# Kernel optimization log

Hardware: AMD Instinct MI355X
Metric: run time of the kernel (lower is better)

## Reference

```python
import jax, jax.numpy as jnp
import numpy as np

B, S, QW, HID, HEADS = 1, 4096, 512, 512, 8
D = HID // HEADS  # size_per_head = 64
SCALE = 1.0 / np.sqrt(float(D))


def setup_inputs() -> dict:
    key = jax.random.key(0)
    k1, k2, k3, k4, k5 = jax.random.split(key, 5)
    return {
        "tensor_q": jax.random.normal(k1, (B, S, QW), dtype=jnp.float32),
        "tensor_k": jax.random.normal(k2, (B, S, QW), dtype=jnp.float32),
        "tensor_v": jax.random.normal(k3, (B, S, QW), dtype=jnp.float32),
        # in_proj_layer: [3*hidden, q_width] (torch uses rand uniform init; randn fine for reference)
        "in_proj": jax.random.normal(k4, (3 * HID, QW), dtype=jnp.float32) * 0.02,
        # out_proj: nn.Linear(hidden, out, bias=False) weight shape [out, hidden]
        "w_out": jax.random.normal(k5, (HID, HID), dtype=jnp.float32) * 0.02,
    }


def reference(tensor_q, tensor_k, tensor_v, in_proj, w_out):
    b, s, _ = tensor_q.shape
    wq, wk, wv = in_proj[:HID], in_proj[HID:2 * HID], in_proj[2 * HID:]
    # mm(W, x_2d^T)^T  ==  x_2d @ W^T ; reshape to [b, s, heads, d]
    q = (tensor_q.reshape(-1, QW) @ wq.T).reshape(b, s, HEADS, D)
    k = (tensor_k.reshape(-1, QW) @ wk.T).reshape(b, s, HEADS, D)
    v = (tensor_v.reshape(-1, QW) @ wv.T).reshape(b, s, HEADS, D)
    # scores: [b, h, s_q, s_k], explicitly materialized as in the source
    scores = jnp.einsum('bqhd,bkhd->bhqk', q, k) * SCALE
    probs = jax.nn.softmax(scores, axis=-1)
    ctx = jnp.einsum('bhqk,bkhd->bqhd', probs, v).reshape(b * s, HID)
    out = ctx @ w_out.T
    return out.reshape(b, s, HID)
```

## Files before the change

kernel.cpp:

```cpp
#include <hip/hip_runtime.h>
#include <hip/hip_bf16.h>

#define S_LEN 4096
#define QW_K  512
#define HID_N 512
#define HEADS 8
#define DH    64
#define QSCALE (0.125f * 1.4426950408889634f)

typedef _Float16 f16;
typedef _Float16 half8  __attribute__((ext_vector_type(8)));
typedef _Float16 half4v __attribute__((ext_vector_type(4)));
typedef float    float4v __attribute__((ext_vector_type(4)));
typedef float    f32x16 __attribute__((ext_vector_type(16)));
typedef unsigned int uint;
typedef unsigned int uint4v __attribute__((ext_vector_type(4)));

__device__ inline uint pkh(float a, float b) {
    return __builtin_bit_cast(uint, __builtin_amdgcn_cvt_pkrtz(a, b));
}
__device__ inline void plswap(uint& a, uint& b) {
    asm volatile("v_permlane32_swap_b32 %0, %1" : "+v"(a), "+v"(b));
}
__device__ inline float hexp2(float x) {
    float r;
    asm("v_exp_f32 %0, %1" : "=v"(r) : "v"(x));
    return r;
}
__device__ __forceinline__ int swz(int s) {
    return (s & 56) | ((s ^ (s >> 3)) & 7);
}


__global__ __launch_bounds__(256) void proj_kernel(
    const float* __restrict__ xq, const float* __restrict__ xk,
    const float* __restrict__ xv, const float* __restrict__ in_proj,
    f16* __restrict__ qws, f16* __restrict__ kws, f16* __restrict__ vtws)
{
    __shared__ f16 As[128][40];
    __shared__ f16 Ws[128][40];

    const int tid  = threadIdx.x;
    const int lane = tid & 63;
    const int w    = tid >> 6;
    const int wm   = w >> 1, wn = w & 1;
    const int l15  = lane & 15, g = lane >> 4;
    const int m0   = blockIdx.x * 128;
    const int n0   = blockIdx.y * 128;
    const int matid = n0 >> 9;
    const float* A = (matid == 0) ? xq : (matid == 1) ? xk : xv;

    float4v acc[4][4];
    for (int i = 0; i < 4; i++)
        for (int j = 0; j < 4; j++)
            for (int r = 0; r < 4; r++) acc[i][j][r] = 0.0f;

    const int srow = tid >> 3;
    const int scol = (tid & 7) * 4;

    for (int k0 = 0; k0 < QW_K; k0 += 32) {
        __syncthreads();
        #pragma unroll
        for (int p = 0; p < 4; p++) {
            int r = p * 32 + srow;
            float4v av = *(const float4v*)(A + (size_t)(m0 + r) * QW_K + k0 + scol);
            float4v wv = *(const float4v*)(in_proj + (size_t)(n0 + r) * QW_K + k0 + scol);
            half4v ah, wh;
            for (int e = 0; e < 4; e++) { ah[e] = (f16)av[e]; wh[e] = (f16)wv[e]; }
            *(half4v*)&As[r][scol] = ah;
            *(half4v*)&Ws[r][scol] = wh;
        }
        __syncthreads();

        half8 a[4], b[4];
        #pragma unroll
        for (int i = 0; i < 4; i++) a[i] = *(const half8*)&As[wm * 64 + i * 16 + l15][g * 8];
        #pragma unroll
        for (int j = 0; j < 4; j++) b[j] = *(const half8*)&Ws[wn * 64 + j * 16 + l15][g * 8];
        #pragma unroll
        for (int i = 0; i < 4; i++)
            #pragma unroll
            for (int j = 0; j < 4; j++)
                acc[i][j] = __builtin_amdgcn_mfma_f32_16x16x32_f16(a[i], b[j], acc[i][j], 0, 0, 0);
    }

    #pragma unroll
    for (int i = 0; i < 4; i++) {
        int grow0 = m0 + wm * 64 + i * 16 + g * 4;
        #pragma unroll
        for (int j = 0; j < 4; j++) {
            int gcol = n0 + wn * 64 + j * 16 + l15;
            int c = gcol & 511;
            int h = c >> 6, d = c & 63;
            if (matid == 2) {
                int db = d >> 5, l31v = d & 31;
                int kb16 = grow0 >> 4;
                int g5v  = (grow0 >> 3) & 1;
                int e0   = grow0 & 7;
                half4v pv;
                for (int r = 0; r < 4; r++) pv[r] = (f16)acc[i][j][r];
                *(half4v*)(vtws + ((size_t)((h * 2 + db) * 256 + kb16) << 9)
                                + l31v * 16 + g5v * 8 + e0) = pv;
            } else if (matid == 0) {
                for (int r = 0; r < 4; r++)
                    qws[((size_t)h * S_LEN + grow0 + r) * DH + d] = (f16)(acc[i][j][r] * QSCALE);
            } else {
                int dblk = d >> 4, g5k = (d >> 3) & 1, e = d & 7;
                for (int r = 0; r < 4; r++) {
                    int s = grow0 + r;
                    kws[((size_t)((h * 128 + (s >> 5)) * 4 + dblk) << 9)
                        + (s & 31) * 16 + g5k * 8 + e] = (f16)acc[i][j][r];
                }
            }
        }
    }
}

__global__ __launch_bounds__(256) void attn_kernel(
    const f16* __restrict__ qws, const f16* __restrict__ kws,
    const f16* __restrict__ vtws, float* __restrict__ ctxws)
{
    __shared__ f16 Kl[8][512];
    __shared__ f16 Vl[8][512];

    const int tid  = threadIdx.x;
    const int lane = tid & 63;
    const int w    = tid >> 6;
    const int l31  = lane & 31;
    const int g5   = lane >> 5;
    const int blk  = blockIdx.x;
    const int h    = blk & 7;
    const int qb   = blk >> 3;
    const int q0   = qb * 128 + w * 32;

    const f16* Kf = kws  + (((size_t)h * 512) << 9);
    const f16* Vf = vtws + (((size_t)h * 512) << 9);
    const int swr = swz(lane) * 8;
    const int srd = swz(2 * l31 + g5) * 8;

    half8 qf[4];
    {
        const f16* qp = qws + ((size_t)h * S_LEN + q0 + l31) * DH + g5 * 8;
        #pragma unroll
        for (int dblk = 0; dblk < 4; dblk++)
            qf[dblk] = *(const half8*)(qp + dblk * 16);
    }

    float lsum = 0.0f;
    f32x16 oacc0, oacc1;
    #pragma unroll
    for (int i = 0; i < 16; i++) { oacc0[i] = 0.0f; oacc1[i] = 0.0f; }

    const int c0 = w * 2;
    half8 kst[2], vst[2];
    #pragma unroll
    for (int i = 0; i < 2; i++) {
        const int c = c0 + i;
        kst[i] = *(const half8*)(Kf + ((size_t)(((c >> 2)) * 4 + (c & 3)) << 9) + lane * 8);
        vst[i] = *(const half8*)(Vf + ((size_t)(((c >> 2) << 8) + (c & 3)) << 9) + lane * 8);
    }

    for (int t = 0; t < 64; t++) {
        __syncthreads();
        #pragma unroll
        for (int i = 0; i < 2; i++) {
            *(half8*)&Kl[c0 + i][swr] = kst[i];
            *(half8*)&Vl[c0 + i][swr] = vst[i];
        }
        if (t + 1 < 64) {
            const int kt = (t + 1) * 2, kb16 = (t + 1) * 4;
            #pragma unroll
            for (int i = 0; i < 2; i++) {
                const int c = c0 + i;
                kst[i] = *(const half8*)(Kf
                    + ((size_t)((kt + (c >> 2)) * 4 + (c & 3)) << 9) + lane * 8);
                vst[i] = *(const half8*)(Vf
                    + ((size_t)(((c >> 2) << 8) + kb16 + (c & 3)) << 9) + lane * 8);
            }
        }
        __syncthreads();

        half8 kf0[4], kf1[4], vf0[4], vf1[4];
        #pragma unroll
        for (int d = 0; d < 4; d++) {
            kf0[d] = *(const half8*)&Kl[d][srd];
            kf1[d] = *(const half8*)&Kl[4 + d][srd];
        }
        #pragma unroll
        for (int k = 0; k < 4; k++) {
            vf0[k] = *(const half8*)&Vl[k][srd];
            vf1[k] = *(const half8*)&Vl[4 + k][srd];
        }

        f32x16 st0, st1;
        #pragma unroll
        for (int i = 0; i < 16; i++) { st0[i] = 0.0f; st1[i] = 0.0f; }
        __builtin_amdgcn_s_setprio(1);
        #pragma unroll
        for (int dblk = 0; dblk < 4; dblk++) {
            st0 = __builtin_amdgcn_mfma_f32_32x32x16_f16(kf0[dblk], qf[dblk], st0, 0, 0, 0);
            st1 = __builtin_amdgcn_mfma_f32_32x32x16_f16(kf1[dblk], qf[dblk], st1, 0, 0, 0);
        }
        __builtin_amdgcn_s_setprio(0);

        #pragma unroll
        for (int i = 0; i < 16; i++) {
            st0[i] = hexp2(st0[i]);
            st1[i] = hexp2(st1[i]);
        }

        f32x16 ss;
        #pragma unroll
        for (int i = 0; i < 16; i++) ss[i] = st0[i] + st1[i];
        #pragma unroll
        for (int off = 8; off >= 1; off >>= 1)
            #pragma unroll
            for (int i = 0; i < off; i++) ss[i] += ss[i + off];
        lsum += ss[0];

        half8 pf[4];
        #pragma unroll
        for (int kb = 0; kb < 2; kb++) {
            uint w0 = pkh(st0[8 * kb + 0], st0[8 * kb + 1]);
            uint w1 = pkh(st0[8 * kb + 2], st0[8 * kb + 3]);
            uint w2 = pkh(st0[8 * kb + 4], st0[8 * kb + 5]);
            uint w3 = pkh(st0[8 * kb + 6], st0[8 * kb + 7]);
            plswap(w0, w2);
            plswap(w1, w3);
            uint4v u; u[0] = w0; u[1] = w1; u[2] = w2; u[3] = w3;
            pf[kb] = __builtin_bit_cast(half8, u);
        }
        #pragma unroll
        for (int kb = 0; kb < 2; kb++) {
            uint w0 = pkh(st1[8 * kb + 0], st1[8 * kb + 1]);
            uint w1 = pkh(st1[8 * kb + 2], st1[8 * kb + 3]);
            uint w2 = pkh(st1[8 * kb + 4], st1[8 * kb + 5]);
            uint w3 = pkh(st1[8 * kb + 6], st1[8 * kb + 7]);
            plswap(w0, w2);
            plswap(w1, w3);
            uint4v u; u[0] = w0; u[1] = w1; u[2] = w2; u[3] = w3;
            pf[2 + kb] = __builtin_bit_cast(half8, u);
        }

        __builtin_amdgcn_s_setprio(1);
        #pragma unroll
        for (int kb = 0; kb < 4; kb++) {
            oacc0 = __builtin_amdgcn_mfma_f32_32x32x16_f16(vf0[kb], pf[kb], oacc0, 0, 0, 0);
            oacc1 = __builtin_amdgcn_mfma_f32_32x32x16_f16(vf1[kb], pf[kb], oacc1, 0, 0, 0);
        }
        __builtin_amdgcn_s_setprio(0);
    }

    lsum += __shfl_xor(lsum, 32);
    const float inv = 1.0f / lsum;
    float* cbase = ctxws + (size_t)(q0 + l31) * HID_N + h * DH;
    #pragma unroll
    for (int rg = 0; rg < 4; rg++) {
        float4v v0, v1;
        #pragma unroll
        for (int j = 0; j < 4; j++) {
            v0[j] = oacc0[rg * 4 + j] * inv;
            v1[j] = oacc1[rg * 4 + j] * inv;
        }
        const int dd = rg * 8 + g5 * 4;
        *(float4v*)(cbase + dd)      = v0;
        *(float4v*)(cbase + 32 + dd) = v1;
    }
}

__global__ __launch_bounds__(256) void outproj_kernel(
    const float* __restrict__ ctxws, const float* __restrict__ w_out,
    float* __restrict__ out)
{
    __shared__ f16 As[128][40];
    __shared__ f16 Ws[128][40];

    const int tid  = threadIdx.x;
    const int lane = tid & 63;
    const int w    = tid >> 6;
    const int wm   = w >> 1, wn = w & 1;
    const int l15  = lane & 15, g = lane >> 4;
    const int m0   = blockIdx.x * 128;
    const int n0   = blockIdx.y * 128;

    float4v acc[4][4];
    for (int i = 0; i < 4; i++)
        for (int j = 0; j < 4; j++)
            for (int r = 0; r < 4; r++) acc[i][j][r] = 0.0f;

    const int srow = tid >> 3;
    const int scol = (tid & 7) * 4;

    for (int k0 = 0; k0 < HID_N; k0 += 32) {
        __syncthreads();
        #pragma unroll
        for (int p = 0; p < 4; p++) {
            int r = p * 32 + srow;
            float4v av = *(const float4v*)(ctxws + (size_t)(m0 + r) * HID_N + k0 + scol);
            float4v wv = *(const float4v*)(w_out + (size_t)(n0 + r) * HID_N + k0 + scol);
            half4v ah, wh;
            for (int e = 0; e < 4; e++) { ah[e] = (f16)av[e]; wh[e] = (f16)wv[e]; }
            *(half4v*)&As[r][scol] = ah;
            *(half4v*)&Ws[r][scol] = wh;
        }
        __syncthreads();

        half8 a[4], b[4];
        #pragma unroll
        for (int i = 0; i < 4; i++) a[i] = *(const half8*)&As[wm * 64 + i * 16 + l15][g * 8];
        #pragma unroll
        for (int j = 0; j < 4; j++) b[j] = *(const half8*)&Ws[wn * 64 + j * 16 + l15][g * 8];
        #pragma unroll
        for (int i = 0; i < 4; i++)
            #pragma unroll
            for (int j = 0; j < 4; j++)
                acc[i][j] = __builtin_amdgcn_mfma_f32_16x16x32_f16(a[i], b[j], acc[i][j], 0, 0, 0);
    }

    #pragma unroll
    for (int i = 0; i < 4; i++) {
        int grow0 = m0 + wm * 64 + i * 16 + g * 4;
        #pragma unroll
        for (int j = 0; j < 4; j++) {
            int gcol = n0 + wn * 64 + j * 16 + l15;
            for (int r = 0; r < 4; r++)
                out[(size_t)(grow0 + r) * HID_N + gcol] = acc[i][j][r];
        }
    }
}

extern "C" void kernel_launch(void* const* d_in, const int* in_sizes, int n_in,
                              void* d_out, int out_size, void* d_ws, size_t ws_size,
                              hipStream_t stream)
{
    const float* xq      = (const float*)d_in[0];
    const float* xk      = (const float*)d_in[1];
    const float* xv      = (const float*)d_in[2];
    const float* in_proj = (const float*)d_in[3];
    const float* w_out   = (const float*)d_in[4];
    float* out = (float*)d_out;

    const size_t per = (size_t)HEADS * S_LEN * DH;
    f16* qws   = (f16*)d_ws;
    f16* kws   = qws + per;
    f16* vtws  = kws + per;
    float* ctxws = (float*)(vtws + per);

    proj_kernel<<<dim3(32, 12), 256, 0, stream>>>(xq, xk, xv, in_proj, qws, kws, vtws);
    attn_kernel<<<dim3(256), 256, 0, stream>>>(qws, kws, vtws, ctxws);
    outproj_kernel<<<dim3(32, 4), 256, 0, stream>>>(ctxws, w_out, out);
}
```

Measured before the change: 110.3 us.

## Split attention KV range across two blocks and merge partials in out-projection

Each (query tile, head) now gets two thread blocks, each covering half of the key/value sequence. Both write unnormalized context partials and row sums to separate buffers, and the out-projection kernel adds them and divides before the fp16 conversion. This doubles the block count so each CU holds more resident waves and can hide more latency. The cost is extra global traffic for the second fp32 context buffer and the row-sum arrays. The LDS write/read pattern is also changed from an XOR swizzle to a lane-pair interleave with linear reads, which may change bank-conflict behaviour.

```diff
diff --git a/kernel.cpp b/kernel.cpp
--- a/kernel.cpp
+++ b/kernel.cpp
@@ -26,9 +26,6 @@
     float r;
     asm("v_exp_f32 %0, %1" : "=v"(r) : "v"(x));
     return r;
-}
-__device__ __forceinline__ int swz(int s) {
-    return (s & 56) | ((s ^ (s >> 3)) & 7);
 }
 
 
@@ -118,7 +115,8 @@
 
 __global__ __launch_bounds__(256) void attn_kernel(
     const f16* __restrict__ qws, const f16* __restrict__ kws,
-    const f16* __restrict__ vtws, float* __restrict__ ctxws)
+    const f16* __restrict__ vtws, float* __restrict__ ctx0,
+    float* __restrict__ ctx1, float* __restrict__ L0, float* __restrict__ L1)
 {
     __shared__ f16 Kl[8][512];
     __shared__ f16 Vl[8][512];
@@ -129,14 +127,14 @@
     const int l31  = lane & 31;
     const int g5   = lane >> 5;
     const int blk  = blockIdx.x;
+    const int kvh  = blk >> 8;
     const int h    = blk & 7;
-    const int qb   = blk >> 3;
+    const int qb   = (blk >> 3) & 31;
     const int q0   = qb * 128 + w * 32;
 
     const f16* Kf = kws  + (((size_t)h * 512) << 9);
     const f16* Vf = vtws + (((size_t)h * 512) << 9);
-    const int swr = swz(lane) * 8;
-    const int srd = swz(2 * l31 + g5) * 8;
+    const int pw = ((lane & 1) * 32 + (lane >> 1)) * 8;
 
     half8 qf[4];
     {
@@ -152,30 +150,33 @@
     for (int i = 0; i < 16; i++) { oacc0[i] = 0.0f; oacc1[i] = 0.0f; }
 
     const int c0 = w * 2;
+    const int T0 = kvh * 32;
     half8 kst[2], vst[2];
     #pragma unroll
     for (int i = 0; i < 2; i++) {
         const int c = c0 + i;
-        kst[i] = *(const half8*)(Kf + ((size_t)(((c >> 2)) * 4 + (c & 3)) << 9) + lane * 8);
-        vst[i] = *(const half8*)(Vf + ((size_t)(((c >> 2) << 8) + (c & 3)) << 9) + lane * 8);
-    }
-
-    for (int t = 0; t < 64; t++) {
+        kst[i] = *(const half8*)(Kf
+            + ((size_t)((T0 * 2 + (c >> 2)) * 4 + (c & 3)) << 9) + lane * 8);
+        vst[i] = *(const half8*)(Vf
+            + ((size_t)(((c >> 2) << 8) + T0 * 4 + (c & 3)) << 9) + lane * 8);
+    }
+
+    for (int t = 0; t < 32; t++) {
         __syncthreads();
         #pragma unroll
         for (int i = 0; i < 2; i++) {
-            *(half8*)&Kl[c0 + i][swr] = kst[i];
-            *(half8*)&Vl[c0 + i][swr] = vst[i];
-        }
-        if (t + 1 < 64) {
-            const int kt = (t + 1) * 2, kb16 = (t + 1) * 4;
+            *(half8*)&Kl[c0 + i][pw] = kst[i];
+            *(half8*)&Vl[c0 + i][pw] = vst[i];
+        }
+        if (t + 1 < 32) {
+            const int T = T0 + t + 1;
             #pragma unroll
             for (int i = 0; i < 2; i++) {
                 const int c = c0 + i;
                 kst[i] = *(const half8*)(Kf
-                    + ((size_t)((kt + (c >> 2)) * 4 + (c & 3)) << 9) + lane * 8);
+                    + ((size_t)((T * 2 + (c >> 2)) * 4 + (c & 3)) << 9) + lane * 8);
                 vst[i] = *(const half8*)(Vf
-                    + ((size_t)(((c >> 2) << 8) + kb16 + (c & 3)) << 9) + lane * 8);
+                    + ((size_t)(((c >> 2) << 8) + T * 4 + (c & 3)) << 9) + lane * 8);
             }
         }
         __syncthreads();
@@ -183,13 +184,13 @@
         half8 kf0[4], kf1[4], vf0[4], vf1[4];
         #pragma unroll
         for (int d = 0; d < 4; d++) {
-            kf0[d] = *(const half8*)&Kl[d][srd];
-            kf1[d] = *(const half8*)&Kl[4 + d][srd];
+            kf0[d] = *(const half8*)&Kl[d][lane * 8];
+            kf1[d] = *(const half8*)&Kl[4 + d][lane * 8];
         }
         #pragma unroll
         for (int k = 0; k < 4; k++) {
-            vf0[k] = *(const half8*)&Vl[k][srd];
-            vf1[k] = *(const half8*)&Vl[4 + k][srd];
+            vf0[k] = *(const half8*)&Vl[k][lane * 8];
+            vf1[k] = *(const half8*)&Vl[4 + k][lane * 8];
         }
 
         f32x16 st0, st1;
@@ -252,25 +253,28 @@
     }
 
     lsum += __shfl_xor(lsum, 32);
-    const float inv = 1.0f / lsum;
-    float* cbase = ctxws + (size_t)(q0 + l31) * HID_N + h * DH;
+    float* cx = kvh ? ctx1 : ctx0;
+    float* Lx = kvh ? L1 : L0;
+    float* cbase = cx + (size_t)(q0 + l31) * HID_N + h * DH;
     #pragma unroll
     for (int rg = 0; rg < 4; rg++) {
         float4v v0, v1;
         #pragma unroll
         for (int j = 0; j < 4; j++) {
-            v0[j] = oacc0[rg * 4 + j] * inv;
-            v1[j] = oacc1[rg * 4 + j] * inv;
+            v0[j] = oacc0[rg * 4 + j];
+            v1[j] = oacc1[rg * 4 + j];
         }
         const int dd = rg * 8 + g5 * 4;
         *(float4v*)(cbase + dd)      = v0;
         *(float4v*)(cbase + 32 + dd) = v1;
     }
+    if (g5 == 0) Lx[(q0 + l31) * 8 + h] = lsum;
 }
 
 __global__ __launch_bounds__(256) void outproj_kernel(
-    const float* __restrict__ ctxws, const float* __restrict__ w_out,
-    float* __restrict__ out)
+    const float* __restrict__ ctx0, const float* __restrict__ ctx1,
+    const float* __restrict__ L0, const float* __restrict__ L1,
+    const float* __restrict__ w_out, float* __restrict__ out)
 {
     __shared__ f16 As[128][40];
     __shared__ f16 Ws[128][40];
@@ -293,13 +297,20 @@
 
     for (int k0 = 0; k0 < HID_N; k0 += 32) {
         __syncthreads();
+        const int hh = (k0 + scol) >> 6;
         #pragma unroll
         for (int p = 0; p < 4; p++) {
             int r = p * 32 + srow;
-            float4v av = *(const float4v*)(ctxws + (size_t)(m0 + r) * HID_N + k0 + scol);
+            int s = m0 + r;
+            float4v a0 = *(const float4v*)(ctx0 + (size_t)s * HID_N + k0 + scol);
+            float4v a1 = *(const float4v*)(ctx1 + (size_t)s * HID_N + k0 + scol);
+            float inv = 1.0f / (L0[s * 8 + hh] + L1[s * 8 + hh]);
             float4v wv = *(const float4v*)(w_out + (size_t)(n0 + r) * HID_N + k0 + scol);
             half4v ah, wh;
-            for (int e = 0; e < 4; e++) { ah[e] = (f16)av[e]; wh[e] = (f16)wv[e]; }
+            for (int e = 0; e < 4; e++) {
+                ah[e] = (f16)((a0[e] + a1[e]) * inv);
+                wh[e] = (f16)wv[e];
+            }
             *(half4v*)&As[r][scol] = ah;
             *(half4v*)&Ws[r][scol] = wh;
         }
@@ -344,9 +355,12 @@
     f16* qws   = (f16*)d_ws;
     f16* kws   = qws + per;
     f16* vtws  = kws + per;
-    float* ctxws = (float*)(vtws + per);
+    float* ctx0 = (float*)(vtws + per);
+    float* ctx1 = ctx0 + (size_t)S_LEN * HID_N;
+    float* L0   = ctx1 + (size_t)S_LEN * HID_N;
+    float* L1   = L0 + (size_t)S_LEN * HEADS;
 
     proj_kernel<<<dim3(32, 12), 256, 0, stream>>>(xq, xk, xv, in_proj, qws, kws, vtws);
-    attn_kernel<<<dim3(256), 256, 0, stream>>>(qws, kws, vtws, ctxws);
-    outproj_kernel<<<dim3(32, 4), 256, 0, stream>>>(ctxws, w_out, out);
-}
+    attn_kernel<<<dim3(512), 256, 0, stream>>>(qws, kws, vtws, ctx0, ctx1, L0, L1);
+    outproj_kernel<<<dim3(32, 4), 256, 0, stream>>>(ctx0, ctx1, L0, L1, w_out, out);
+}
```

After: 101.0 us. 1.09x faster.
